# Performance work log

Hardware: AMD Instinct MI355X
Metric: run time of the kernel (lower is better)

Reference implementation:

```python
import jax, jax.numpy as jnp
import numpy as np

N = 100_000   # nodes
E = 3_200_000 # edges (avg degree 32)
F = 256       # in_features == out_features


def setup_inputs() -> dict:
    key = jax.random.key(0)
    k1, k2, k3, k4, k5, k6 = jax.random.split(key, 6)
    x = jax.random.normal(k1, (N, F), dtype=jnp.float32)
    h0 = jax.random.normal(k2, (N, F), dtype=jnp.float32)
    adj_rows = jax.random.randint(k3, (E,), 0, N, dtype=jnp.int32)
    adj_cols = jax.random.randint(k4, (E,), 0, N, dtype=jnp.int32)
    # roughly row-normalized adjacency values (avg degree 32)
    adj_vals = jax.random.uniform(k5, (E,), dtype=jnp.float32) / 32.0
    stdv = 1.0 / np.sqrt(F)
    weight = jax.random.uniform(k6, (F, F), dtype=jnp.float32, minval=-stdv, maxval=stdv)
    return {"x": x, "adj_rows": adj_rows, "adj_cols": adj_cols, "adj_vals": adj_vals,
            "h0": h0, "weight": weight, "lamda": 0.5, "alpha": 0.1, "l": 4}


def reference(x, adj_rows, adj_cols, adj_vals, h0, weight, lamda, alpha, l):
    # theta = log(lamda/l + 1)
    theta = jnp.log(jnp.float32(lamda) / l + 1.0)
    # hi = sparse.mm(adj, x): gather source rows, scale by edge value, scatter-add to dest rows
    hi = jax.ops.segment_sum(adj_vals[:, None] * x[adj_cols], adj_rows, num_segments=x.shape[0])  # [N, F]
    # support == 1 branch: affine blend with initial features h0
    support = (1.0 - alpha) * hi + alpha * h0
    # output = theta * support @ W + (1 - theta) * support   (residual=False)
    return theta * (support @ weight) + (1.0 - theta) * support
```

## Files before the change

kernel.cpp:

```cpp
#include <hip/hip_runtime.h>
#include <math.h>

#define F 256

#define BKT_SHIFT 7
#define BKT_ROWS 128
#define BKT_CAP 8192
#define NB_MAX 1024
#define BIN_CHUNK 8192

typedef __attribute__((ext_vector_type(8))) short short8;
typedef __attribute__((ext_vector_type(4))) float f32x4;
typedef __attribute__((ext_vector_type(2))) int i32x2;
typedef __attribute__((ext_vector_type(4))) unsigned short u16x4;
typedef __attribute__((ext_vector_type(8))) unsigned short u16x8;

__device__ __forceinline__ unsigned short f2bf(float f) {
  union { float f; unsigned u; } v; v.f = f;
  unsigned r = (v.u + 0x7fffu + ((v.u >> 16) & 1u)) >> 16;
  return (unsigned short)r;
}
__device__ __forceinline__ float bf2f(unsigned short h) {
  union { unsigned u; float f; } v; v.u = ((unsigned)h) << 16;
  return v.f;
}

__global__ void prep(const float* __restrict__ W, unsigned short* __restrict__ Wt,
                     const float* __restrict__ x, unsigned short* __restrict__ xb,
                     int NF, int do_xb) {
  if (blockIdx.x < 256) {
    int idx = blockIdx.x * 256 + threadIdx.x;
    int k = idx >> 8, n = idx & 255;
    Wt[n * F + k] = f2bf(W[k * F + n]);
    return;
  }
  if (!do_xb) return;
  int i0 = (blockIdx.x - 256) * 2048 + threadIdx.x * 8;
  if (i0 + 8 <= NF) {
    f32x4 a = __builtin_nontemporal_load((const f32x4*)(x + i0));
    f32x4 b = __builtin_nontemporal_load((const f32x4*)(x + i0 + 4));
    u16x8 o;
    o[0] = f2bf(a.x); o[1] = f2bf(a.y); o[2] = f2bf(a.z); o[3] = f2bf(a.w);
    o[4] = f2bf(b.x); o[5] = f2bf(b.y); o[6] = f2bf(b.z); o[7] = f2bf(b.w);
    *(u16x8*)(xb + i0) = o;
  } else {
    for (int i = i0; i < NF; ++i) xb[i] = f2bf(x[i]);
  }
}

__global__ void hist_rows(const int* __restrict__ rows, int* counts, int E) {
  int e = blockIdx.x * 256 + threadIdx.x;
  if (e < E) atomicAdd(&counts[__builtin_nontemporal_load(&rows[e])], 1);
}

__global__ void scan1(const int* __restrict__ counts, int* row_start, int* blk, int N) {
  __shared__ int tmp[256];
  int t = threadIdx.x;
  int i = blockIdx.x * 256 + t;
  int v = (i < N) ? counts[i] : 0;
  tmp[t] = v;
  __syncthreads();
#pragma unroll
  for (int off = 1; off < 256; off <<= 1) {
    int a = (t >= off) ? tmp[t - off] : 0;
    __syncthreads();
    tmp[t] += a;
    __syncthreads();
  }
  if (i < N) row_start[i] = tmp[t] - v;
  if (t == 255) blk[blockIdx.x] = tmp[255];
}

__global__ void scan2(int* blk, int NB) {
  __shared__ int tmp[512];
  int t = threadIdx.x;
  int v = (t < NB) ? blk[t] : 0;
  tmp[t] = v;
  __syncthreads();
#pragma unroll
  for (int off = 1; off < 512; off <<= 1) {
    int a = (t >= off) ? tmp[t - off] : 0;
    __syncthreads();
    tmp[t] += a;
    __syncthreads();
  }
  if (t < NB) blk[t] = tmp[t] - v;
}

__global__ void scan3(const int* __restrict__ counts, int* row_start,
                      const int* __restrict__ blk, int* fill_ptr, int* bcur, int N) {
  int i = blockIdx.x * 256 + threadIdx.x;
  if (i >= N) return;
  int rs = row_start[i] + blk[i >> 8];
  row_start[i] = rs;
  fill_ptr[i] = rs;
  if ((i & (BKT_ROWS - 1)) == 0) bcur[i >> BKT_SHIFT] = rs;
  if (i == N - 1) row_start[N] = rs + counts[i];
}

__global__ void fill_csr(const int* __restrict__ rows, const int* __restrict__ cols,
                         const float* __restrict__ vals, int* fill_ptr,
                         int2* __restrict__ edges, int E) {
  int e = blockIdx.x * 256 + threadIdx.x;
  if (e >= E) return;
  int r = __builtin_nontemporal_load(&rows[e]);
  int c = __builtin_nontemporal_load(&cols[e]);
  float v = __builtin_nontemporal_load(&vals[e]);
  int pos = atomicAdd(&fill_ptr[r], 1);
  edges[pos] = make_int2(c, __float_as_int(v));
}

__global__ __launch_bounds__(512) void bin_edges(
    const int* __restrict__ rows, const int* __restrict__ cols,
    const float* __restrict__ vals, int* __restrict__ bcur,
    i32x2* __restrict__ etmp, int E, int NB) {
  __shared__ unsigned hist[NB_MAX];
  __shared__ unsigned base[NB_MAX];
  const int tid = threadIdx.x;
  const int e0 = blockIdx.x * BIN_CHUNK;

  for (int b = tid; b < NB; b += 512) hist[b] = 0;
  __syncthreads();
#pragma unroll
  for (int k = 0; k < BIN_CHUNK / 512; ++k) {
    int e = e0 + k * 512 + tid;
    if (e < E) {
      unsigned b = (unsigned)__builtin_nontemporal_load(&rows[e]) >> BKT_SHIFT;
      atomicAdd(&hist[b], 1u);
    }
  }
  __syncthreads();
  for (int b = tid; b < NB; b += 512) {
    unsigned c = hist[b];
    base[b] = c ? (unsigned)atomicAdd(&bcur[b], (int)c) : 0u;
    hist[b] = 0;
  }
  __syncthreads();
#pragma unroll
  for (int k = 0; k < BIN_CHUNK / 512; ++k) {
    int e = e0 + k * 512 + tid;
    if (e < E) {
      int r = rows[e];
      unsigned b = (unsigned)r >> BKT_SHIFT;
      unsigned idx = atomicAdd(&hist[b], 1u);
      int pos = (int)(base[b] + idx);
      int c = cols[e];
      float v = vals[e];
      etmp[pos] = (i32x2){c | ((r & (BKT_ROWS - 1)) << 20), __float_as_int(v)};
    }
  }
}

__global__ __launch_bounds__(512) void sort_bucket(
    const i32x2* __restrict__ etmp, const int* __restrict__ row_start,
    int* __restrict__ fill_ptr, i32x2* __restrict__ edges, int N) {
  __shared__ int cur[BKT_ROWS];
  __shared__ i32x2 sorted[BKT_CAP];
  const int b = blockIdx.x;
  const int r0 = b << BKT_SHIFT;
  int rend = r0 + BKT_ROWS; if (rend > N) rend = N;
  const int seg0 = row_start[r0];
  const int seg1 = row_start[rend];
  const int cnt = seg1 - seg0;
  const int tid = threadIdx.x;

  if (cnt <= BKT_CAP) {
    if (tid < BKT_ROWS) cur[tid] = 0;
    __syncthreads();
    for (int i = tid; i < cnt; i += 512) {
      i32x2 w = etmp[seg0 + i];
      atomicAdd(&cur[(w.x >> 20) & (BKT_ROWS - 1)], 1);
    }
    __syncthreads();
    int myc = (tid < BKT_ROWS) ? cur[tid] : 0;
    __syncthreads();
    for (int off = 1; off < BKT_ROWS; off <<= 1) {
      int a = 0;
      if (tid < BKT_ROWS && tid >= off) a = cur[tid - off];
      __syncthreads();
      if (tid < BKT_ROWS) cur[tid] += a;
      __syncthreads();
    }
    if (tid < BKT_ROWS) cur[tid] -= myc;
    __syncthreads();
    for (int i = tid; i < cnt; i += 512) {
      i32x2 w = etmp[seg0 + i];
      int rl = (w.x >> 20) & (BKT_ROWS - 1);
      int idx = atomicAdd(&cur[rl], 1);
      sorted[idx] = (i32x2){w.x & 0xFFFFF, w.y};
    }
    __syncthreads();
    for (int i = tid; i < cnt; i += 512)
      edges[seg0 + i] = sorted[i];
  } else {
    for (int i = tid; i < cnt; i += 512) {
      i32x2 w = etmp[seg0 + i];
      int r = r0 + ((w.x >> 20) & (BKT_ROWS - 1));
      int pos = atomicAdd(&fill_ptr[r], 1);
      edges[pos] = (i32x2){w.x & 0xFFFFF, w.y};
    }
  }
}

__global__ __launch_bounds__(256) void gather_rows_bf16(
    const unsigned short* __restrict__ xb, const float* __restrict__ h0,
    const int* __restrict__ row_start, const i32x2* __restrict__ edges,
    float* __restrict__ support, const float* __restrict__ alpha_p, int N) {
  int gid = blockIdx.x * 256 + threadIdx.x;
  int r = gid >> 6;
  if (r >= N) return;
  int lane = threadIdx.x & 63;
  float alpha = *alpha_p;
  int s = row_start[r], e = row_start[r + 1];

  const unsigned short* xbl = xb + lane * 4;

  f32x4 acc0 = (f32x4){0.f, 0.f, 0.f, 0.f};
  f32x4 acc1 = (f32x4){0.f, 0.f, 0.f, 0.f};

#define GRP_LOAD(XV, VV, JB)                                             \
  {                                                                      \
    _Pragma("unroll")                                                    \
    for (int k = 0; k < 8; ++k) {                                        \
      int col = __builtin_amdgcn_readlane(med.x, (JB) + k);              \
      VV[k] = __int_as_float(__builtin_amdgcn_readlane(med.y, (JB) + k)); \
      XV[k] = *(const u16x4*)(xbl + (size_t)col * F);                    \
    }                                                                    \
  }

#define GRP_FMA(XV, VV)                                                  \
  {                                                                      \
    _Pragma("unroll")                                                    \
    for (int k = 0; k < 8; ++k) {                                        \
      f32x4& A = (k & 1) ? acc1 : acc0;                                  \
      A.x += VV[k] * bf2f(XV[k][0]);                                     \
      A.y += VV[k] * bf2f(XV[k][1]);                                     \
      A.z += VV[k] * bf2f(XV[k][2]);                                     \
      A.w += VV[k] * bf2f(XV[k][3]);                                     \
    }                                                                    \
  }

  while (s < e) {
    int cnt = e - s;
    if (cnt > 64) cnt = 64;

    i32x2 med;
    if (lane < cnt) {
      med = edges[s + lane];
    } else {
      med.x = 0; med.y = 0;
    }

    u16x4 xA[8], xB[8];
    float vA[8], vB[8];

    int jb = 0;
    GRP_LOAD(xA, vA, 0);
    while (true) {
      int jn = jb + 8;
      if (jn < cnt) GRP_LOAD(xB, vB, jn);
      GRP_FMA(xA, vA);
      jb = jn;
      if (jb >= cnt) break;
      jn = jb + 8;
      if (jn < cnt) GRP_LOAD(xA, vA, jn);
      GRP_FMA(xB, vB);
      jb = jn;
      if (jb >= cnt) break;
    }
    s += cnt;
  }
#undef GRP_LOAD
#undef GRP_FMA

  f32x4 acc = acc0 + acc1;
  f32x4 b = __builtin_nontemporal_load((const f32x4*)(h0 + (size_t)r * F) + lane);
  float om = 1.0f - alpha;
  f32x4 o = om * acc + alpha * b;
  *((f32x4*)(support + (size_t)r * F) + lane) = o;
}

__global__ __launch_bounds__(256) void gather_rows_f32(
    const float* __restrict__ x, const float* __restrict__ h0,
    const int* __restrict__ row_start, const i32x2* __restrict__ edges,
    float* __restrict__ support, const float* __restrict__ alpha_p, int N) {
  int gid = blockIdx.x * 256 + threadIdx.x;
  int r = gid >> 6;
  if (r >= N) return;
  int lane = threadIdx.x & 63;
  float alpha = *alpha_p;
  int s = row_start[r], e = row_start[r + 1];
  f32x4 acc = (f32x4){0.f, 0.f, 0.f, 0.f};
  if (s < e) {
    i32x2 ed = __builtin_nontemporal_load(&edges[s]);
    f32x4 xv = *((const f32x4*)(x + (size_t)ed.x * F) + lane);
    for (int j = s; j < e; ++j) {
      i32x2 cur = ed;
      f32x4 xc = xv;
      if (j + 1 < e) {
        ed = __builtin_nontemporal_load(&edges[j + 1]);
        xv = *((const f32x4*)(x + (size_t)ed.x * F) + lane);
      }
      float v = __int_as_float(cur.y);
      acc += v * xc;
    }
  }
  f32x4 b = __builtin_nontemporal_load((const f32x4*)(h0 + (size_t)r * F) + lane);
  float om = 1.0f - alpha;
  f32x4 o = om * acc + alpha * b;
  *((f32x4*)(support + (size_t)r * F) + lane) = o;
}

__global__ __launch_bounds__(256) void gemm_epilogue(
    const float* support, const unsigned short* __restrict__ Wt, float* out,
    const float* __restrict__ lamda_p, const int* __restrict__ l_p, int N) {
  __shared__ unsigned short sup[64][264];

  const float theta = logf(*lamda_p / (float)(*l_p) + 1.0f);
  const float one_m_t = 1.0f - theta;

  const int m0 = blockIdx.x * 64;
  const int t = threadIdx.x;

#pragma unroll
  for (int i = 0; i < 16; ++i) {
    int f = t + i * 256;
    int row = f >> 6, c4 = f & 63;
    int g_row = m0 + row;
    f32x4 a = (f32x4){0.f, 0.f, 0.f, 0.f};
    if (g_row < N)
      a = __builtin_nontemporal_load((const f32x4*)(support + (size_t)g_row * F) + c4);
    unsigned short* p = &sup[row][c4 << 2];
    p[0] = f2bf(a.x); p[1] = f2bf(a.y); p[2] = f2bf(a.z); p[3] = f2bf(a.w);
  }
  __syncthreads();

  const int wave = t >> 6, lane = t & 63;
  const int quad = lane >> 4, lcol = lane & 15;
  const int mrow = wave * 16;

  f32x4 acc[16];
#pragma unroll
  for (int n = 0; n < 16; ++n) acc[n] = (f32x4){0.f, 0.f, 0.f, 0.f};

#pragma unroll
  for (int k = 0; k < 8; ++k) {
    short8 afrag = *(const short8*)&sup[mrow + lcol][k * 32 + quad * 8];
#pragma unroll
    for (int n = 0; n < 16; ++n) {
      short8 bfrag = *(const short8*)&Wt[(size_t)(n * 16 + lcol) * F + k * 32 + quad * 8];
      acc[n] = __builtin_amdgcn_mfma_f32_16x16x32_bf16(afrag, bfrag, acc[n], 0, 0, 0);
    }
  }

#pragma unroll
  for (int n = 0; n < 16; ++n) {
#pragma unroll
    for (int r = 0; r < 4; ++r) {
      int lrow = mrow + quad * 4 + r;
      int col = n * 16 + lcol;
      int g_row = m0 + lrow;
      if (g_row < N) {
        float s = bf2f(sup[lrow][col]);
        __builtin_nontemporal_store(theta * acc[n][r] + one_m_t * s,
                                    &out[(size_t)g_row * F + col]);
      }
    }
  }
}

extern "C" void kernel_launch(void* const* d_in, const int* in_sizes, int n_in,
                              void* d_out, int out_size, void* d_ws, size_t ws_size,
                              hipStream_t stream) {
  const float* x     = (const float*)d_in[0];
  const int*   rows  = (const int*)d_in[1];
  const int*   cols  = (const int*)d_in[2];
  const float* vals  = (const float*)d_in[3];
  const float* h0    = (const float*)d_in[4];
  const float* W     = (const float*)d_in[5];
  const float* lamda = (const float*)d_in[6];
  const float* alpha = (const float*)d_in[7];
  const int*   lp    = (const int*)d_in[8];

  const int E = in_sizes[1];
  const int N = in_sizes[0] / F;
  const int NF = N * F;
  const int NB = (N + BKT_ROWS - 1) >> BKT_SHIFT;

  size_t off = 0;
  auto take = [&](size_t bytes) { size_t o = off; off += (bytes + 255) & ~(size_t)255; return o; };
  char* ws = (char*)d_ws;
  unsigned short* Wt  = (unsigned short*)(ws + take((size_t)F * F * 2));
  int* counts    = (int*)(ws + take((size_t)N * 4));
  int* row_start = (int*)(ws + take((size_t)(N + 1) * 4));
  int* fill_ptr  = (int*)(ws + take((size_t)N * 4));
  int* blk       = (int*)(ws + take(4096));
  int* bcur      = (int*)(ws + take(4096));
  i32x2* edges   = (i32x2*)(ws + take((size_t)E * 8));
  unsigned short* xb = (unsigned short*)(ws + take((size_t)NF * 2));
  const int use_bf16 = (off <= ws_size);

  float* out = (float*)d_out;

  const int use_sort = (N <= (1 << 20)) && (NB <= NB_MAX) &&
                       ((size_t)E * 8 <= (size_t)out_size);

  hipMemsetAsync(counts, 0, (size_t)N * sizeof(int), stream);

  int nxb = use_bf16 ? (NF + 2047) / 2048 : 0;
  prep<<<256 + nxb, 256, 0, stream>>>(W, Wt, x, xb, NF, use_bf16);

  int eb = (E + 255) / 256;
  int nb = (N + 255) / 256;

  hist_rows<<<eb, 256, 0, stream>>>(rows, counts, E);
  scan1<<<nb, 256, 0, stream>>>(counts, row_start, blk, N);
  scan2<<<1, 512, 0, stream>>>(blk, nb);
  scan3<<<nb, 256, 0, stream>>>(counts, row_start, blk, fill_ptr, bcur, N);

  if (use_sort) {
    i32x2* etmp = (i32x2*)out;
    bin_edges<<<(E + BIN_CHUNK - 1) / BIN_CHUNK, 512, 0, stream>>>(
        rows, cols, vals, bcur, etmp, E, NB);
    sort_bucket<<<NB, 512, 0, stream>>>(etmp, row_start, fill_ptr, edges, N);
  } else {
    fill_csr<<<eb, 256, 0, stream>>>(rows, cols, vals, fill_ptr, (int2*)edges, E);
  }

  int gather_blocks = (N * 64 + 255) / 256;
  if (use_bf16) {
    gather_rows_bf16<<<gather_blocks, 256, 0, stream>>>(xb, h0, row_start, edges,
                                                        out, alpha, N);
  } else {
    gather_rows_f32<<<gather_blocks, 256, 0, stream>>>(x, h0, row_start, edges,
                                                       out, alpha, N);
  }

  gemm_epilogue<<<(N + 63) / 64, 256, 0, stream>>>(out, Wt, out, lamda, lp, N);
}
```

Before: 833.0 us.

## Replace per-row histogram with bucket-level counts and deepen gather prefetch

The sort path no longer builds a global per-row histogram and three-pass scan. It counts edges per 128-row bucket with shared-memory histograms, scans those bucket counts in a single block, and lets sort_bucket compute each row's start offset locally, writing row_start itself. This drops a full-E global atomic histogram pass and several launches. The bf16 gather kernel also now loads 16 neighbours per group instead of 8, with a fixed unrolled schedule up to 64 edges, which raises memory-level parallelism at the cost of more registers.

```diff
diff --git a/kernel.cpp b/kernel.cpp
--- a/kernel.cpp
+++ b/kernel.cpp
@@ -88,13 +88,12 @@
 }
 
 __global__ void scan3(const int* __restrict__ counts, int* row_start,
-                      const int* __restrict__ blk, int* fill_ptr, int* bcur, int N) {
+                      const int* __restrict__ blk, int* fill_ptr, int N) {
   int i = blockIdx.x * 256 + threadIdx.x;
   if (i >= N) return;
   int rs = row_start[i] + blk[i >> 8];
   row_start[i] = rs;
   fill_ptr[i] = rs;
-  if ((i & (BKT_ROWS - 1)) == 0) bcur[i >> BKT_SHIFT] = rs;
   if (i == N - 1) row_start[N] = rs + counts[i];
 }
 
@@ -110,6 +109,52 @@
   edges[pos] = make_int2(c, __float_as_int(v));
 }
 
+__global__ __launch_bounds__(512) void bin_count(
+    const int* __restrict__ rows, int* __restrict__ bucket_counts, int E, int NB) {
+  __shared__ unsigned hist[NB_MAX];
+  const int tid = threadIdx.x;
+  const int e0 = blockIdx.x * BIN_CHUNK;
+  for (int b = tid; b < NB; b += 512) hist[b] = 0;
+  __syncthreads();
+#pragma unroll
+  for (int k = 0; k < BIN_CHUNK / 512; ++k) {
+    int e = e0 + k * 512 + tid;
+    if (e < E) {
+      unsigned b = (unsigned)__builtin_nontemporal_load(&rows[e]) >> BKT_SHIFT;
+      atomicAdd(&hist[b], 1u);
+    }
+  }
+  __syncthreads();
+  for (int b = tid; b < NB; b += 512)
+    if (hist[b]) atomicAdd(&bucket_counts[b], (int)hist[b]);
+}
+
+__global__ __launch_bounds__(1024) void scan_buckets(
+    const int* __restrict__ bucket_counts, int* __restrict__ bbase,
+    int* __restrict__ bcur, int* __restrict__ row_start, int NB, int N, int E) {
+  __shared__ int tmp[1024];
+  int t = threadIdx.x;
+  int v = (t < NB) ? bucket_counts[t] : 0;
+  tmp[t] = v;
+  __syncthreads();
+#pragma unroll
+  for (int off = 1; off < 1024; off <<= 1) {
+    int a = (t >= off) ? tmp[t - off] : 0;
+    __syncthreads();
+    tmp[t] += a;
+    __syncthreads();
+  }
+  if (t < NB) {
+    int ex = tmp[t] - v;
+    bbase[t] = ex;
+    bcur[t] = ex;
+  }
+  if (t == 0) {
+    bbase[NB] = E;
+    row_start[N] = E;
+  }
+}
+
 __global__ __launch_bounds__(512) void bin_edges(
     const int* __restrict__ rows, const int* __restrict__ cols,
     const float* __restrict__ vals, int* __restrict__ bcur,
@@ -152,37 +197,43 @@
 }
 
 __global__ __launch_bounds__(512) void sort_bucket(
-    const i32x2* __restrict__ etmp, const int* __restrict__ row_start,
-    int* __restrict__ fill_ptr, i32x2* __restrict__ edges, int N) {
+    const i32x2* __restrict__ etmp, const int* __restrict__ bbase,
+    i32x2* __restrict__ edges, int* __restrict__ row_start, int N) {
   __shared__ int cur[BKT_ROWS];
+  __shared__ int pre[BKT_ROWS];
   __shared__ i32x2 sorted[BKT_CAP];
   const int b = blockIdx.x;
   const int r0 = b << BKT_SHIFT;
-  int rend = r0 + BKT_ROWS; if (rend > N) rend = N;
-  const int seg0 = row_start[r0];
-  const int seg1 = row_start[rend];
-  const int cnt = seg1 - seg0;
+  int nrows = N - r0; if (nrows > BKT_ROWS) nrows = BKT_ROWS;
+  const int seg0 = bbase[b];
+  const int cnt = bbase[b + 1] - seg0;
   const int tid = threadIdx.x;
 
+  if (tid < BKT_ROWS) cur[tid] = 0;
+  __syncthreads();
+  for (int i = tid; i < cnt; i += 512) {
+    i32x2 w = etmp[seg0 + i];
+    atomicAdd(&cur[(w.x >> 20) & (BKT_ROWS - 1)], 1);
+  }
+  __syncthreads();
+  int myc = (tid < BKT_ROWS) ? cur[tid] : 0;
+  __syncthreads();
+  for (int off = 1; off < BKT_ROWS; off <<= 1) {
+    int a = 0;
+    if (tid < BKT_ROWS && tid >= off) a = cur[tid - off];
+    __syncthreads();
+    if (tid < BKT_ROWS) cur[tid] += a;
+    __syncthreads();
+  }
+  if (tid < BKT_ROWS) {
+    int ex = cur[tid] - myc;
+    pre[tid] = ex;
+    cur[tid] = ex;
+    if (tid < nrows) row_start[r0 + tid] = seg0 + ex;
+  }
+  __syncthreads();
+
   if (cnt <= BKT_CAP) {
-    if (tid < BKT_ROWS) cur[tid] = 0;
-    __syncthreads();
-    for (int i = tid; i < cnt; i += 512) {
-      i32x2 w = etmp[seg0 + i];
-      atomicAdd(&cur[(w.x >> 20) & (BKT_ROWS - 1)], 1);
-    }
-    __syncthreads();
-    int myc = (tid < BKT_ROWS) ? cur[tid] : 0;
-    __syncthreads();
-    for (int off = 1; off < BKT_ROWS; off <<= 1) {
-      int a = 0;
-      if (tid < BKT_ROWS && tid >= off) a = cur[tid - off];
-      __syncthreads();
-      if (tid < BKT_ROWS) cur[tid] += a;
-      __syncthreads();
-    }
-    if (tid < BKT_ROWS) cur[tid] -= myc;
-    __syncthreads();
     for (int i = tid; i < cnt; i += 512) {
       i32x2 w = etmp[seg0 + i];
       int rl = (w.x >> 20) & (BKT_ROWS - 1);
@@ -195,9 +246,9 @@
   } else {
     for (int i = tid; i < cnt; i += 512) {
       i32x2 w = etmp[seg0 + i];
-      int r = r0 + ((w.x >> 20) & (BKT_ROWS - 1));
-      int pos = atomicAdd(&fill_ptr[r], 1);
-      edges[pos] = (i32x2){w.x & 0xFFFFF, w.y};
+      int rl = (w.x >> 20) & (BKT_ROWS - 1);
+      int idx = atomicAdd(&cur[rl], 1);
+      edges[seg0 + idx] = (i32x2){w.x & 0xFFFFF, w.y};
     }
   }
 }
@@ -218,26 +269,26 @@
   f32x4 acc0 = (f32x4){0.f, 0.f, 0.f, 0.f};
   f32x4 acc1 = (f32x4){0.f, 0.f, 0.f, 0.f};
 
-#define GRP_LOAD(XV, VV, JB)                                             \
-  {                                                                      \
-    _Pragma("unroll")                                                    \
-    for (int k = 0; k < 8; ++k) {                                        \
-      int col = __builtin_amdgcn_readlane(med.x, (JB) + k);              \
+#define GRP_LOAD16(XV, VV, JB)                                            \
+  {                                                                       \
+    _Pragma("unroll")                                                     \
+    for (int k = 0; k < 16; ++k) {                                        \
+      int col = __builtin_amdgcn_readlane(med.x, (JB) + k);               \
       VV[k] = __int_as_float(__builtin_amdgcn_readlane(med.y, (JB) + k)); \
-      XV[k] = *(const u16x4*)(xbl + (size_t)col * F);                    \
-    }                                                                    \
-  }
-
-#define GRP_FMA(XV, VV)                                                  \
-  {                                                                      \
-    _Pragma("unroll")                                                    \
-    for (int k = 0; k < 8; ++k) {                                        \
-      f32x4& A = (k & 1) ? acc1 : acc0;                                  \
-      A.x += VV[k] * bf2f(XV[k][0]);                                     \
-      A.y += VV[k] * bf2f(XV[k][1]);                                     \
-      A.z += VV[k] * bf2f(XV[k][2]);                                     \
-      A.w += VV[k] * bf2f(XV[k][3]);                                     \
-    }                                                                    \
+      XV[k] = *(const u16x4*)(xbl + (size_t)col * F);                     \
+    }                                                                     \
+  }
+
+#define GRP_FMA16(XV, VV)                                                 \
+  {                                                                       \
+    _Pragma("unroll")                                                     \
+    for (int k = 0; k < 16; ++k) {                                        \
+      f32x4& A = (k & 1) ? acc1 : acc0;                                   \
+      A.x += VV[k] * bf2f(XV[k][0]);                                      \
+      A.y += VV[k] * bf2f(XV[k][1]);                                      \
+      A.z += VV[k] * bf2f(XV[k][2]);                                      \
+      A.w += VV[k] * bf2f(XV[k][3]);                                      \
+    }                                                                     \
   }
 
   while (s < e) {
@@ -251,27 +302,25 @@
       med.x = 0; med.y = 0;
     }
 
-    u16x4 xA[8], xB[8];
-    float vA[8], vB[8];
-
-    int jb = 0;
-    GRP_LOAD(xA, vA, 0);
-    while (true) {
-      int jn = jb + 8;
-      if (jn < cnt) GRP_LOAD(xB, vB, jn);
-      GRP_FMA(xA, vA);
-      jb = jn;
-      if (jb >= cnt) break;
-      jn = jb + 8;
-      if (jn < cnt) GRP_LOAD(xA, vA, jn);
-      GRP_FMA(xB, vB);
-      jb = jn;
-      if (jb >= cnt) break;
+    u16x4 xA[16], xB[16];
+    float vA[16], vB[16];
+
+    GRP_LOAD16(xA, vA, 0);
+    if (cnt > 16) GRP_LOAD16(xB, vB, 16);
+    GRP_FMA16(xA, vA);
+    if (cnt > 16) {
+      if (cnt > 32) GRP_LOAD16(xA, vA, 32);
+      GRP_FMA16(xB, vB);
+      if (cnt > 32) {
+        if (cnt > 48) GRP_LOAD16(xB, vB, 48);
+        GRP_FMA16(xA, vA);
+        if (cnt > 48) GRP_FMA16(xB, vB);
+      }
     }
     s += cnt;
   }
-#undef GRP_LOAD
-#undef GRP_FMA
+#undef GRP_LOAD16
+#undef GRP_FMA16
 
   f32x4 acc = acc0 + acc1;
   f32x4 b = __builtin_nontemporal_load((const f32x4*)(h0 + (size_t)r * F) + lane);
@@ -395,7 +444,9 @@
   int* row_start = (int*)(ws + take((size_t)(N + 1) * 4));
   int* fill_ptr  = (int*)(ws + take((size_t)N * 4));
   int* blk       = (int*)(ws + take(4096));
-  int* bcur      = (int*)(ws + take(4096));
+  int* bucket_counts = (int*)(ws + take((size_t)NB_MAX * 4));
+  int* bbase     = (int*)(ws + take((size_t)(NB_MAX + 1) * 4));
+  int* bcur      = (int*)(ws + take((size_t)NB_MAX * 4));
   i32x2* edges   = (i32x2*)(ws + take((size_t)E * 8));
   unsigned short* xb = (unsigned short*)(ws + take((size_t)NF * 2));
   const int use_bf16 = (off <= ws_size);
@@ -405,25 +456,27 @@
   const int use_sort = (N <= (1 << 20)) && (NB <= NB_MAX) &&
                        ((size_t)E * 8 <= (size_t)out_size);
 
-  hipMemsetAsync(counts, 0, (size_t)N * sizeof(int), stream);
-
   int nxb = use_bf16 ? (NF + 2047) / 2048 : 0;
   prep<<<256 + nxb, 256, 0, stream>>>(W, Wt, x, xb, NF, use_bf16);
 
   int eb = (E + 255) / 256;
   int nb = (N + 255) / 256;
-
-  hist_rows<<<eb, 256, 0, stream>>>(rows, counts, E);
-  scan1<<<nb, 256, 0, stream>>>(counts, row_start, blk, N);
-  scan2<<<1, 512, 0, stream>>>(blk, nb);
-  scan3<<<nb, 256, 0, stream>>>(counts, row_start, blk, fill_ptr, bcur, N);
+  int bchunks = (E + BIN_CHUNK - 1) / BIN_CHUNK;
 
   if (use_sort) {
     i32x2* etmp = (i32x2*)out;
-    bin_edges<<<(E + BIN_CHUNK - 1) / BIN_CHUNK, 512, 0, stream>>>(
-        rows, cols, vals, bcur, etmp, E, NB);
-    sort_bucket<<<NB, 512, 0, stream>>>(etmp, row_start, fill_ptr, edges, N);
+    hipMemsetAsync(bucket_counts, 0, (size_t)NB * sizeof(int), stream);
+    bin_count<<<bchunks, 512, 0, stream>>>(rows, bucket_counts, E, NB);
+    scan_buckets<<<1, 1024, 0, stream>>>(bucket_counts, bbase, bcur, row_start,
+                                         NB, N, E);
+    bin_edges<<<bchunks, 512, 0, stream>>>(rows, cols, vals, bcur, etmp, E, NB);
+    sort_bucket<<<NB, 512, 0, stream>>>(etmp, bbase, edges, row_start, N);
   } else {
+    hipMemsetAsync(counts, 0, (size_t)N * sizeof(int), stream);
+    hist_rows<<<eb, 256, 0, stream>>>(rows, counts, E);
+    scan1<<<nb, 256, 0, stream>>>(counts, row_start, blk, N);
+    scan2<<<1, 512, 0, stream>>>(blk, nb);
+    scan3<<<nb, 256, 0, stream>>>(counts, row_start, blk, fill_ptr, N);
     fill_csr<<<eb, 256, 0, stream>>>(rows, cols, vals, fill_ptr, (int2*)edges, E);
   }
 
```

Result: faster. 711.6 us (-14.6%).
